# Kernel tuning notes

Hardware: AMD Instinct MI355X
Metric: run time of the kernel (lower is better)

## Reference

```python
import jax, jax.numpy as jnp
import numpy as np

BN_EPS = 1e-5


def setup_inputs() -> dict:
    key = jax.random.key(0)
    k1, k2, k3, k4 = jax.random.split(key, 4)
    B, C_in, T, V = 64, 64, 300, 25
    K, C_out = 3, 64
    x = jax.random.normal(k1, (B, C_in, T, V), dtype=jnp.float32)
    # 1x1 Conv2d weight collapsed to (K*C_out, C_in); bias (K*C_out,)
    W = jax.random.normal(k2, (K * C_out, C_in), dtype=jnp.float32) * (1.0 / np.sqrt(C_in))
    b = jax.random.normal(k3, (K * C_out,), dtype=jnp.float32) * 0.02
    A = jax.random.uniform(k4, (K, V, V), dtype=jnp.float32)
    gamma = jnp.ones((C_out,), dtype=jnp.float32)
    beta = jnp.zeros((C_out,), dtype=jnp.float32)
    return {"x": x, "W": W, "b": b, "A": A, "gamma": gamma, "beta": beta}


def reference(x, W, b, A, gamma, beta):
    B, C_in, T, V = x.shape
    K = A.shape[0]
    C_out = W.shape[0] // K
    # 1x1 conv == per-pixel matmul over channels
    x_conv = jnp.einsum('bctv,oc->botv', x, W) + b[None, :, None, None]
    # split into K partitions: (B, K, C_out, T, V)
    x_conv = x_conv.reshape(B, K, C_out, T, V)
    # fused per-partition graph matmul + sum over partitions
    out = jnp.einsum('bkctv,kvw->bctw', x_conv, A)
    # BatchNorm2d (training mode: batch statistics over B, T, V)
    mean = jnp.mean(out, axis=(0, 2, 3), keepdims=True)
    var = jnp.var(out, axis=(0, 2, 3), keepdims=True)  # biased variance
    out_hat = (out - mean) * jax.lax.rsqrt(var + BN_EPS)
    return out_hat * gamma[None, :, None, None] + beta[None, :, None, None]
```

## Files before the change

kernel.cpp:

```cpp
#include <hip/hip_runtime.h>
#include <stdint.h>


#define TT 3
#define NPIX (TT * 25)
#define NT1 5
#define NBLK 6400
#define XSTRIDE 68
#define TSZ 4800

typedef short bf16x8 __attribute__((ext_vector_type(8)));
typedef float f32x4 __attribute__((ext_vector_type(4)));

union frag_u { bf16x8 v; uint32_t u[4]; };

__device__ inline short f2bf(float f) {
    union { float f; uint32_t u; } v; v.f = f;
    uint32_t u = v.u;
    u += 0x7fffu + ((u >> 16) & 1u);
    return (short)(u >> 16);
}

__device__ inline uint32_t cvtpk(float lo, float hi) {
    uint32_t d;
    asm("v_cvt_pk_bf16_f32 %0, %1, %2" : "=v"(d) : "v"(lo), "v"(hi));
    return d;
}

__device__ inline short f2h(float f) {
    union { _Float16 h; short s; } u; u.h = (_Float16)f; return u.s;
}
__device__ inline float h2f(short s) {
    union { short s; _Float16 h; } u; u.s = s; return (float)u.h;
}

__global__ __launch_bounds__(256, 4) void sgc_main(
    const float* __restrict__ x, const float* __restrict__ W,
    const float* __restrict__ bias, const float* __restrict__ A,
    short* __restrict__ ws, float* __restrict__ stats_part)
{
    __shared__ __align__(16) short smem[18432];
    float* xT   = (float*)smem;
    short* Ylds = smem;

    const int tid  = threadIdx.x;
    const int lane = tid & 63;
    const int wave = tid >> 6;
    const int q4   = lane >> 4;
    const int wl   = lane & 15;
    const int bid  = blockIdx.x;
    const int b    = bid / 100;
    const int t0   = (bid % 100) * TT;

    bf16x8 wfrag[3][2];
    #pragma unroll
    for (int k = 0; k < 3; ++k) {
        int o = k * 64 + wave * 16 + wl;
        #pragma unroll
        for (int kb = 0; kb < 2; ++kb) {
            int ci0 = kb * 32 + q4 * 8;
            const float4 f0 = *(const float4*)&W[o * 64 + ci0];
            const float4 f1 = *(const float4*)&W[o * 64 + ci0 + 4];
            frag_u fr;
            fr.u[0] = cvtpk(f0.x, f0.y);
            fr.u[1] = cvtpk(f0.z, f0.w);
            fr.u[2] = cvtpk(f1.x, f1.y);
            fr.u[3] = cvtpk(f1.z, f1.w);
            wfrag[k][kb] = fr.v;
        }
    }

    {
        const float* xg = x + (size_t)b * 480000 + (size_t)t0 * 25 + lane * 7500;
        float4 vv[5];
        int segs[5];
        #pragma unroll
        for (int j = 0; j < 5; ++j) {
            int seg = wave + 4 * j;
            segs[j] = seg;
            if (seg < 18) {
                vv[j] = *(const float4*)(xg + seg * 4);
            } else if (seg == 18) {
                vv[j].x = xg[72]; vv[j].y = xg[73]; vv[j].z = xg[74]; vv[j].w = 0.f;
            }
        }
        #pragma unroll
        for (int j = 0; j < 5; ++j) {
            int seg = segs[j];
            if (seg < 19) {
                int px0 = seg * 4;
                xT[(px0 + 0) * XSTRIDE + lane] = vv[j].x;
                xT[(px0 + 1) * XSTRIDE + lane] = vv[j].y;
                xT[(px0 + 2) * XSTRIDE + lane] = vv[j].z;
                if (seg < 18) xT[(px0 + 3) * XSTRIDE + lane] = vv[j].w;
            }
        }
    }

    __syncthreads();

    f32x4 acc[3][NT1];
    #pragma unroll
    for (int k = 0; k < 3; ++k)
        #pragma unroll
        for (int nt = 0; nt < NT1; ++nt) {
            f32x4 zf = {0.f, 0.f, 0.f, 0.f};
            acc[k][nt] = zf;
        }

    #pragma unroll
    for (int nt = 0; nt < NT1; ++nt) {
        int px = nt * 16 + wl;
        if (px > 74) px = 74;
        const float* row = &xT[px * XSTRIDE + q4 * 8];
        float4 q0 = *(const float4*)&row[0];
        float4 q1 = *(const float4*)&row[4];
        float4 q2 = *(const float4*)&row[32];
        float4 q3 = *(const float4*)&row[36];
        frag_u x0, x1;
        x0.u[0] = cvtpk(q0.x, q0.y); x0.u[1] = cvtpk(q0.z, q0.w);
        x0.u[2] = cvtpk(q1.x, q1.y); x0.u[3] = cvtpk(q1.z, q1.w);
        x1.u[0] = cvtpk(q2.x, q2.y); x1.u[1] = cvtpk(q2.z, q2.w);
        x1.u[2] = cvtpk(q3.x, q3.y); x1.u[3] = cvtpk(q3.z, q3.w);
        #pragma unroll
        for (int k = 0; k < 3; ++k) {
            acc[k][nt] = __builtin_amdgcn_mfma_f32_16x16x32_bf16(
                wfrag[k][0], x0.v, acc[k][nt], 0, 0, 0);
            acc[k][nt] = __builtin_amdgcn_mfma_f32_16x16x32_bf16(
                wfrag[k][1], x1.v, acc[k][nt], 0, 0, 0);
        }
    }

    __syncthreads();

    const int wbase = wave * 4608;

    #pragma unroll
    for (int tile = 0; tile < 9; ++tile)
        *(int*)&Ylds[wbase + tile * 512 + 384 + lane * 2] = 0;

    float4 bv[3];
    #pragma unroll
    for (int k = 0; k < 3; ++k)
        bv[k] = *(const float4*)&bias[k * 64 + wave * 16 + q4 * 4];

    #pragma unroll
    for (int nt = 0; nt < NT1; ++nt) {
        int n = nt * 16 + wl;
        if (n < NPIX) {
            int t = n / 25, v = n - t * 25;
            #pragma unroll
            for (int k = 0; k < 3; ++k) {
                int base = wbase + (t * 3 + k) * 512
                         + (v >> 3) * 128 + q4 * 32 + (v & 7);
                const float* bp = (const float*)&bv[k];
                #pragma unroll
                for (int r = 0; r < 4; ++r)
                    Ylds[base + r * 8] = f2bf(acc[k][nt][r] + bp[r]);
            }
        }
    }

    bf16x8 bfrag2[2][3];
    #pragma unroll
    for (int nt2 = 0; nt2 < 2; ++nt2) {
        int w = nt2 * 16 + wl;
        #pragma unroll
        for (int kb2 = 0; kb2 < 3; ++kb2) {
            frag_u fr;
            #pragma unroll
            for (int p = 0; p < 4; ++p) {
                int v0 = q4 * 8 + 2 * p;
                float a0 = (w < 25 && v0     < 25) ? A[(kb2 * 25 + v0) * 25 + w]     : 0.f;
                float a1 = (w < 25 && v0 + 1 < 25) ? A[(kb2 * 25 + v0 + 1) * 25 + w] : 0.f;
                fr.u[p] = cvtpk(a0, a1);
            }
            bfrag2[nt2][kb2] = fr.v;
        }
    }

    float ssum[4] = {0.f, 0.f, 0.f, 0.f};
    float ssq[4]  = {0.f, 0.f, 0.f, 0.f};
    short* wstile = ws + (size_t)bid * TSZ;
    const int cl0 = q4 * 4;
    const int c0  = wave * 16 + cl0;

    #pragma unroll
    for (int t = 0; t < TT; ++t) {
        bf16x8 a2[3];
        #pragma unroll
        for (int kb2 = 0; kb2 < 3; ++kb2)
            a2[kb2] = *(const bf16x8*)&Ylds[wbase + (t * 3 + kb2) * 512 + lane * 8];

        f32x4 acc2[2];
        #pragma unroll
        for (int nt2 = 0; nt2 < 2; ++nt2) {
            f32x4 zf = {0.f, 0.f, 0.f, 0.f};
            acc2[nt2] = zf;
            #pragma unroll
            for (int kb2 = 0; kb2 < 3; ++kb2)
                acc2[nt2] = __builtin_amdgcn_mfma_f32_16x16x32_bf16(
                    a2[kb2], bfrag2[nt2][kb2], acc2[nt2], 0, 0, 0);
        }

        #pragma unroll
        for (int nt2 = 0; nt2 < 2; ++nt2) {
            int w = nt2 * 16 + wl;
            bool valid = (w < 25);
            #pragma unroll
            for (int r = 0; r < 4; ++r) {
                float val = acc2[nt2][r];
                if (valid) {
                    wstile[(c0 + r) * 75 + t * 25 + w] = f2h(val);
                    ssum[r] += val;
                    ssq[r]  += val * val;
                }
            }
        }
    }

    #pragma unroll
    for (int r = 0; r < 4; ++r) {
        float s = ssum[r], q = ssq[r];
        #pragma unroll
        for (int d = 1; d < 16; d <<= 1) {
            s += __shfl_xor(s, d);
            q += __shfl_xor(q, d);
        }
        if (wl == 0) {
            int c = c0 + r;
            int slot = bid & 63;
            atomicAdd(&stats_part[slot * 128 + c], s);
            atomicAdd(&stats_part[slot * 128 + 64 + c], q);
        }
    }
}

__global__ void sgc_finalize(const float* __restrict__ stats_part,
                             const float* __restrict__ gamma,
                             const float* __restrict__ beta,
                             float* __restrict__ scaleshift)
{
    int c = threadIdx.x;
    float s = 0.f, q = 0.f;
    #pragma unroll 8
    for (int slot = 0; slot < 64; ++slot) {
        s += stats_part[slot * 128 + c];
        q += stats_part[slot * 128 + 64 + c];
    }
    const float invN = 1.f / 480000.f;
    float mean = s * invN;
    float var  = q * invN - mean * mean;
    float rstd = rsqrtf(var + 1e-5f);
    float sc = rstd * gamma[c];
    scaleshift[c]      = sc;
    scaleshift[64 + c] = beta[c] - mean * sc;
}

__global__ __launch_bounds__(256) void sgc_normws(
    const short* __restrict__ ws, const float* __restrict__ scaleshift,
    float* __restrict__ out)
{
    const int bid   = blockIdx.x;
    const int b     = bid / 100;
    const int chunk = bid % 100;
    const short* tile = ws + (size_t)bid * TSZ;
    float* ob = out + (size_t)b * 480000 + (size_t)chunk * NPIX;

    #pragma unroll
    for (int j = 0; j < 19; ++j) {
        int i = threadIdx.x + 256 * j;
        if (i < 4800) {
            int c = i / 75;
            int r = i - c * 75;
            float y = h2f(tile[i]);
            ob[c * 7500 + r] = y * scaleshift[c] + scaleshift[64 + c];
        }
    }
}

__global__ __launch_bounds__(256, 3) void sgc_main_fb(
    const float* __restrict__ x, const float* __restrict__ W,
    const float* __restrict__ bias, const float* __restrict__ A,
    float* __restrict__ out, float* __restrict__ stats_part)
{
    __shared__ __align__(16) short Ylds[18432];
    __shared__ __align__(16) short Acat[3072];

    const int tid  = threadIdx.x;
    const int lane = tid & 63;
    const int wave = tid >> 6;
    const int q4   = lane >> 4;
    const int wl   = lane & 15;
    const int bid  = blockIdx.x;
    const int b    = bid / 100;
    const int t0   = (bid % 100) * TT;

    {
        bf16x8 z8 = {0,0,0,0,0,0,0,0};
        #pragma unroll
        for (int j = 0; j < 3; ++j) {
            int s = tid + 256 * j;
            if (s < 576)
                *(bf16x8*)&Ylds[(s >> 4) * 512 + 384 + (s & 15) * 8] = z8;
        }
    }

    #pragma unroll
    for (int j = 0; j < 2; ++j) {
        int g = tid + 256 * j;
        if (g < 384) {
            int tile = g >> 6;
            int kb2  = tile >> 1, nt2 = tile & 1;
            int oct  = (g >> 4) & 3;
            int w    = nt2 * 16 + (g & 15);
            frag_u fr;
            #pragma unroll
            for (int p = 0; p < 4; ++p) {
                int v0 = oct * 8 + 2 * p;
                float a0 = (w < 25 && v0     < 25) ? A[(kb2 * 25 + v0) * 25 + w]     : 0.f;
                float a1 = (w < 25 && v0 + 1 < 25) ? A[(kb2 * 25 + v0 + 1) * 25 + w] : 0.f;
                fr.u[p] = cvtpk(a0, a1);
            }
            *(bf16x8*)&Acat[g * 8] = fr.v;
        }
    }

    bf16x8 wfrag[3][2];
    #pragma unroll
    for (int mti = 0; mti < 3; ++mti) {
        int o = (wave * 3 + mti) * 16 + wl;
        #pragma unroll
        for (int kb = 0; kb < 2; ++kb) {
            int ci0 = kb * 32 + q4 * 8;
            const float4 f0 = *(const float4*)&W[o * 64 + ci0];
            const float4 f1 = *(const float4*)&W[o * 64 + ci0 + 4];
            frag_u fr;
            fr.u[0] = cvtpk(f0.x, f0.y);
            fr.u[1] = cvtpk(f0.z, f0.w);
            fr.u[2] = cvtpk(f1.x, f1.y);
            fr.u[3] = cvtpk(f1.z, f1.w);
            wfrag[mti][kb] = fr.v;
        }
    }

    const float* xp = x + (size_t)b * 480000 + (size_t)t0 * 25;
    f32x4 acc[3][NT1];
    #pragma unroll
    for (int mti = 0; mti < 3; ++mti)
        #pragma unroll
        for (int nt = 0; nt < NT1; ++nt) {
            f32x4 zf = {0.f, 0.f, 0.f, 0.f};
            acc[mti][nt] = zf;
        }

    #pragma unroll
    for (int nt = 0; nt < NT1; ++nt) {
        int n = nt * 16 + wl;
        if (n > NPIX - 1) n = NPIX - 1;
        int loff = q4 * 60000 + n;
        bf16x8 xb[2];
        #pragma unroll
        for (int kb = 0; kb < 2; ++kb) {
            float xv[8];
            #pragma unroll
            for (int jj = 0; jj < 8; ++jj)
                xv[jj] = (xp + (kb * 32 + jj) * 7500)[loff];
            frag_u fr;
            #pragma unroll
            for (int p = 0; p < 4; ++p)
                fr.u[p] = cvtpk(xv[2 * p], xv[2 * p + 1]);
            xb[kb] = fr.v;
        }
        #pragma unroll
        for (int mti = 0; mti < 3; ++mti) {
            acc[mti][nt] = __builtin_amdgcn_mfma_f32_16x16x32_bf16(
                wfrag[mti][0], xb[0], acc[mti][nt], 0, 0, 0);
            acc[mti][nt] = __builtin_amdgcn_mfma_f32_16x16x32_bf16(
                wfrag[mti][1], xb[1], acc[mti][nt], 0, 0, 0);
        }
    }

    float4 bv[3];
    #pragma unroll
    for (int mti = 0; mti < 3; ++mti)
        bv[mti] = *(const float4*)&bias[(wave * 3 + mti) * 16 + q4 * 4];

    __syncthreads();

    #pragma unroll
    for (int nt = 0; nt < NT1; ++nt) {
        int n = nt * 16 + wl;
        if (n < NPIX) {
            int t = n / 25, v = n % 25;
            #pragma unroll
            for (int mti = 0; mti < 3; ++mti) {
                int wt = wave * 3 + mti;
                int k  = wt >> 2, cq = wt & 3;
                int kv = k * 32 + v;
                int sbase = ((t * 4 + cq) * 3 + k) * 512
                          + ((kv >> 3) & 3) * 128 + q4 * 32 + (kv & 7);
                const float* bp = (const float*)&bv[mti];
                #pragma unroll
                for (int r = 0; r < 4; ++r)
                    Ylds[sbase + r * 8] = f2bf(acc[mti][nt][r] + bp[r]);
            }
        }
    }
    __syncthreads();

    bf16x8 bfrag2[2][3];
    #pragma unroll
    for (int nt2 = 0; nt2 < 2; ++nt2)
        #pragma unroll
        for (int kb2 = 0; kb2 < 3; ++kb2)
            bfrag2[nt2][kb2] = *(const bf16x8*)&Acat[((kb2 * 2 + nt2) * 64 + lane) * 8];

    float ssum[4] = {0.f, 0.f, 0.f, 0.f};
    float ssq[4]  = {0.f, 0.f, 0.f, 0.f};
    const int c0 = wave * 16 + q4 * 4;

    #pragma unroll
    for (int t = 0; t < TT; ++t) {
        bf16x8 a2[3];
        #pragma unroll
        for (int kb2 = 0; kb2 < 3; ++kb2)
            a2[kb2] = *(const bf16x8*)&Ylds[(((t * 4 + wave) * 3 + kb2) * 64 + lane) * 8];

        f32x4 acc2[2];
        #pragma unroll
        for (int nt2 = 0; nt2 < 2; ++nt2) {
            f32x4 zf = {0.f, 0.f, 0.f, 0.f};
            acc2[nt2] = zf;
            #pragma unroll
            for (int kb2 = 0; kb2 < 3; ++kb2)
                acc2[nt2] = __builtin_amdgcn_mfma_f32_16x16x32_bf16(
                    a2[kb2], bfrag2[nt2][kb2], acc2[nt2], 0, 0, 0);
        }

        #pragma unroll
        for (int nt2 = 0; nt2 < 2; ++nt2) {
            int w = nt2 * 16 + wl;
            bool valid = (w < 25);
            #pragma unroll
            for (int r = 0; r < 4; ++r) {
                float val = acc2[nt2][r];
                if (valid) {
                    out[(size_t)((b * 64 + c0 + r) * 300 + t0 + t) * 25 + w] = val;
                    ssum[r] += val;
                    ssq[r]  += val * val;
                }
            }
        }
    }

    #pragma unroll
    for (int r = 0; r < 4; ++r) {
        float s = ssum[r], q = ssq[r];
        #pragma unroll
        for (int d = 1; d < 16; d <<= 1) {
            s += __shfl_xor(s, d);
            q += __shfl_xor(q, d);
        }
        if (wl == 0) {
            int c = c0 + r;
            int slot = bid & 63;
            atomicAdd(&stats_part[slot * 128 + c], s);
            atomicAdd(&stats_part[slot * 128 + 64 + c], q);
        }
    }
}

__global__ __launch_bounds__(256) void sgc_norm_fb(float* __restrict__ out,
                                                   const float* __restrict__ scaleshift)
{
    const int total4 = 30720000 / 4;
    int stride = gridDim.x * 256;
    for (int i = blockIdx.x * 256 + threadIdx.x; i < total4; i += stride) {
        int c = (i / 1875) & 63;
        float sc = scaleshift[c], sh = scaleshift[64 + c];
        float4 v = *((float4*)out + i);
        v.x = v.x * sc + sh;
        v.y = v.y * sc + sh;
        v.z = v.z * sc + sh;
        v.w = v.w * sc + sh;
        *((float4*)out + i) = v;
    }
}

extern "C" void kernel_launch(void* const* d_in, const int* in_sizes, int n_in,
                              void* d_out, int out_size, void* d_ws, size_t ws_size,
                              hipStream_t stream)
{
    const float* x     = (const float*)d_in[0];
    const float* W     = (const float*)d_in[1];
    const float* bias  = (const float*)d_in[2];
    const float* A     = (const float*)d_in[3];
    const float* gamma = (const float*)d_in[4];
    const float* beta  = (const float*)d_in[5];
    float* out = (float*)d_out;

    const size_t tile_bytes = (size_t)NBLK * TSZ * sizeof(short);
    const size_t need = tile_bytes + 64 * 128 * sizeof(float) + 128 * sizeof(float);

    if (ws_size >= need) {
        short* tiles      = (short*)d_ws;
        float* stats      = (float*)((char*)d_ws + tile_bytes);
        float* scaleshift = stats + 64 * 128;

        hipMemsetAsync(stats, 0, 64 * 128 * sizeof(float), stream);
        sgc_main<<<NBLK, 256, 0, stream>>>(x, W, bias, A, tiles, stats);
        sgc_finalize<<<1, 64, 0, stream>>>(stats, gamma, beta, scaleshift);
        sgc_normws<<<NBLK, 256, 0, stream>>>(tiles, scaleshift, out);
    } else {
        float* stats      = (float*)d_ws;
        float* scaleshift = stats + 64 * 128;

        hipMemsetAsync(stats, 0, 64 * 128 * sizeof(float), stream);
        sgc_main_fb<<<NBLK, 256, 0, stream>>>(x, W, bias, A, out, stats);
        sgc_finalize<<<1, 64, 0, stream>>>(stats, gamma, beta, scaleshift);
        sgc_norm_fb<<<4096, 256, 0, stream>>>(out, scaleshift);
    }
}
```

Before: 344.2 us.

## Fuse conv, graph matmul, BN stats and normalize into one cooperative persistent kernel

Replaces the three-kernel pipeline (main, finalize, normalize) plus memset with a single cooperative kernel of 1024 persistent blocks. Each block loops over tiles, prefetching the next tile's x into registers while computing the current one. Per-block BN partial sums are written without atomics, then reduced after a grid sync, and a second grid sync precedes the in-kernel normalization pass. This removes launch overhead and atomics, but adds two grid-wide barriers and a normalize phase whose fp16 workspace reads are strided. The fallback path now writes into a workspace region that may be too small, since it runs exactly when ws_size is below the requirement.

Result: slower. 941.6 us (+173.6%).

```diff
diff --git a/kernel.cpp b/kernel.cpp
--- a/kernel.cpp
+++ b/kernel.cpp
@@ -1,11 +1,15 @@
 #include <hip/hip_runtime.h>
+#include <hip/hip_cooperative_groups.h>
 #include <stdint.h>
+
+namespace cg = cooperative_groups;
 
 
 #define TT 3
 #define NPIX (TT * 25)
 #define NT1 5
-#define NBLK 6400
+#define NTILE 6400
+#define GRID 1024
 #define XSTRIDE 68
 #define TSZ 4800
 
@@ -34,10 +38,12 @@
     union { short s; _Float16 h; } u; u.s = s; return (float)u.h;
 }
 
-__global__ __launch_bounds__(256, 4) void sgc_main(
+__global__ __launch_bounds__(256, 4) void sgc_fused(
     const float* __restrict__ x, const float* __restrict__ W,
     const float* __restrict__ bias, const float* __restrict__ A,
-    short* __restrict__ ws, float* __restrict__ stats_part)
+    const float* __restrict__ gamma, const float* __restrict__ beta,
+    float* __restrict__ out, short* __restrict__ ws,
+    float* __restrict__ stats_part, float* __restrict__ chansum)
 {
     __shared__ __align__(16) short smem[18432];
     float* xT   = (float*)smem;
@@ -49,8 +55,6 @@
     const int q4   = lane >> 4;
     const int wl   = lane & 15;
     const int bid  = blockIdx.x;
-    const int b    = bid / 100;
-    const int t0   = (bid % 100) * TT;
 
     bf16x8 wfrag[3][2];
     #pragma unroll
@@ -70,23 +74,53 @@
         }
     }
 
+    bf16x8 bfrag2[2][3];
+    #pragma unroll
+    for (int nt2 = 0; nt2 < 2; ++nt2) {
+        int w = nt2 * 16 + wl;
+        #pragma unroll
+        for (int kb2 = 0; kb2 < 3; ++kb2) {
+            frag_u fr;
+            #pragma unroll
+            for (int p = 0; p < 4; ++p) {
+                int v0 = q4 * 8 + 2 * p;
+                float a0 = (w < 25 && v0     < 25) ? A[(kb2 * 25 + v0) * 25 + w]     : 0.f;
+                float a1 = (w < 25 && v0 + 1 < 25) ? A[(kb2 * 25 + v0 + 1) * 25 + w] : 0.f;
+                fr.u[p] = cvtpk(a0, a1);
+            }
+            bfrag2[nt2][kb2] = fr.v;
+        }
+    }
+
+    float4 bv[3];
+    #pragma unroll
+    for (int k = 0; k < 3; ++k)
+        bv[k] = *(const float4*)&bias[k * 64 + wave * 16 + q4 * 4];
+
+    float ssum[4] = {0.f, 0.f, 0.f, 0.f};
+    float ssq[4]  = {0.f, 0.f, 0.f, 0.f};
+    const int c0 = wave * 16 + q4 * 4;
+
+    float4 vv[5];
     {
+        int tile = bid;
+        int b = tile / 100;
+        int t0 = (tile - b * 100) * TT;
         const float* xg = x + (size_t)b * 480000 + (size_t)t0 * 25 + lane * 7500;
-        float4 vv[5];
-        int segs[5];
         #pragma unroll
         for (int j = 0; j < 5; ++j) {
             int seg = wave + 4 * j;
-            segs[j] = seg;
-            if (seg < 18) {
-                vv[j] = *(const float4*)(xg + seg * 4);
-            } else if (seg == 18) {
-                vv[j].x = xg[72]; vv[j].y = xg[73]; vv[j].z = xg[74]; vv[j].w = 0.f;
-            }
-        }
+            if (seg < 18) vv[j] = *(const float4*)(xg + seg * 4);
+            else if (seg == 18) { vv[j].x = xg[72]; vv[j].y = xg[73]; vv[j].z = xg[74]; vv[j].w = 0.f; }
+        }
+    }
+
+    for (int tile = bid; tile < NTILE; tile += GRID) {
+        __syncthreads();
+
         #pragma unroll
         for (int j = 0; j < 5; ++j) {
-            int seg = segs[j];
+            int seg = wave + 4 * j;
             if (seg < 19) {
                 int px0 = seg * 4;
                 xT[(px0 + 0) * XSTRIDE + lane] = vv[j].x;
@@ -95,8 +129,246 @@
                 if (seg < 18) xT[(px0 + 3) * XSTRIDE + lane] = vv[j].w;
             }
         }
-    }
-
+
+        float4 vv2[5];
+        int ntile = tile + GRID;
+        if (ntile < NTILE) {
+            int b2 = ntile / 100;
+            int t02 = (ntile - b2 * 100) * TT;
+            const float* xg = x + (size_t)b2 * 480000 + (size_t)t02 * 25 + lane * 7500;
+            #pragma unroll
+            for (int j = 0; j < 5; ++j) {
+                int seg = wave + 4 * j;
+                if (seg < 18) vv2[j] = *(const float4*)(xg + seg * 4);
+                else if (seg == 18) { vv2[j].x = xg[72]; vv2[j].y = xg[73]; vv2[j].z = xg[74]; vv2[j].w = 0.f; }
+            }
+        }
+
+        __syncthreads();
+
+        f32x4 acc[3][NT1];
+        #pragma unroll
+        for (int k = 0; k < 3; ++k)
+            #pragma unroll
+            for (int nt = 0; nt < NT1; ++nt) {
+                f32x4 zf = {0.f, 0.f, 0.f, 0.f};
+                acc[k][nt] = zf;
+            }
+
+        #pragma unroll
+        for (int nt = 0; nt < NT1; ++nt) {
+            int px = nt * 16 + wl;
+            if (px > 74) px = 74;
+            const float* row = &xT[px * XSTRIDE + q4 * 8];
+            float4 a0 = *(const float4*)&row[0];
+            float4 a1 = *(const float4*)&row[4];
+            float4 a2 = *(const float4*)&row[32];
+            float4 a3 = *(const float4*)&row[36];
+            frag_u x0, x1;
+            x0.u[0] = cvtpk(a0.x, a0.y); x0.u[1] = cvtpk(a0.z, a0.w);
+            x0.u[2] = cvtpk(a1.x, a1.y); x0.u[3] = cvtpk(a1.z, a1.w);
+            x1.u[0] = cvtpk(a2.x, a2.y); x1.u[1] = cvtpk(a2.z, a2.w);
+            x1.u[2] = cvtpk(a3.x, a3.y); x1.u[3] = cvtpk(a3.z, a3.w);
+            #pragma unroll
+            for (int k = 0; k < 3; ++k) {
+                acc[k][nt] = __builtin_amdgcn_mfma_f32_16x16x32_bf16(
+                    wfrag[k][0], x0.v, acc[k][nt], 0, 0, 0);
+                acc[k][nt] = __builtin_amdgcn_mfma_f32_16x16x32_bf16(
+                    wfrag[k][1], x1.v, acc[k][nt], 0, 0, 0);
+            }
+        }
+
+        __syncthreads();
+
+        const int wbase = wave * 4608;
+
+        #pragma unroll
+        for (int tl = 0; tl < 9; ++tl)
+            *(int*)&Ylds[wbase + tl * 512 + 384 + lane * 2] = 0;
+
+        #pragma unroll
+        for (int nt = 0; nt < NT1; ++nt) {
+            int n = nt * 16 + wl;
+            if (n < NPIX) {
+                int t = n / 25, v = n - t * 25;
+                #pragma unroll
+                for (int k = 0; k < 3; ++k) {
+                    int base = wbase + (t * 3 + k) * 512
+                             + (v >> 3) * 128 + q4 * 32 + (v & 7);
+                    const float* bp = (const float*)&bv[k];
+                    #pragma unroll
+                    for (int r = 0; r < 4; ++r)
+                        Ylds[base + r * 8] = f2bf(acc[k][nt][r] + bp[r]);
+                }
+            }
+        }
+
+        short* wstile = ws + (size_t)tile * TSZ;
+        #pragma unroll
+        for (int t = 0; t < TT; ++t) {
+            bf16x8 a2[3];
+            #pragma unroll
+            for (int kb2 = 0; kb2 < 3; ++kb2)
+                a2[kb2] = *(const bf16x8*)&Ylds[wbase + (t * 3 + kb2) * 512 + lane * 8];
+
+            f32x4 acc2[2];
+            #pragma unroll
+            for (int nt2 = 0; nt2 < 2; ++nt2) {
+                f32x4 zf = {0.f, 0.f, 0.f, 0.f};
+                acc2[nt2] = zf;
+                #pragma unroll
+                for (int kb2 = 0; kb2 < 3; ++kb2)
+                    acc2[nt2] = __builtin_amdgcn_mfma_f32_16x16x32_bf16(
+                        a2[kb2], bfrag2[nt2][kb2], acc2[nt2], 0, 0, 0);
+            }
+
+            #pragma unroll
+            for (int nt2 = 0; nt2 < 2; ++nt2) {
+                int w = nt2 * 16 + wl;
+                bool valid = (w < 25);
+                #pragma unroll
+                for (int r = 0; r < 4; ++r) {
+                    float val = acc2[nt2][r];
+                    if (valid) {
+                        wstile[(c0 + r) * 75 + t * 25 + w] = f2h(val);
+                        ssum[r] += val;
+                        ssq[r]  += val * val;
+                    }
+                }
+            }
+        }
+
+        #pragma unroll
+        for (int j = 0; j < 5; ++j) vv[j] = vv2[j];
+    }
+
+    #pragma unroll
+    for (int r = 0; r < 4; ++r) {
+        float s = ssum[r], q = ssq[r];
+        #pragma unroll
+        for (int d = 1; d < 16; d <<= 1) {
+            s += __shfl_xor(s, d);
+            q += __shfl_xor(q, d);
+        }
+        if (wl == 0) {
+            stats_part[bid * 128 + c0 + r]      = s;
+            stats_part[bid * 128 + 64 + c0 + r] = q;
+        }
+    }
+
+    __threadfence();
+    cg::this_grid().sync();
+
+    if (bid < 64) {
+        float* red = (float*)smem;
+        int m  = 2 * bid + (tid >> 7);
+        int ts = tid & 127;
+        float s = 0.f;
+        #pragma unroll
+        for (int k = 0; k < 8; ++k)
+            s += stats_part[(ts * 8 + k) * 128 + m];
+        red[tid] = s;
+        __syncthreads();
+        #pragma unroll
+        for (int d = 64; d > 0; d >>= 1) {
+            if ((tid & 127) < d) red[tid] += red[tid + d];
+            __syncthreads();
+        }
+        if ((tid & 127) == 0) chansum[m] = red[tid];
+    }
+
+    __threadfence();
+    cg::this_grid().sync();
+
+    const float invN = 1.f / 480000.f;
+    const int Rbase = bid * 4;
+    #pragma unroll
+    for (int rr = 0; rr < 4; ++rr) {
+        int R = Rbase + rr;
+        int b = R >> 6, c = R & 63;
+        float mean = chansum[c] * invN;
+        float var  = chansum[64 + c] * invN - mean * mean;
+        float rstd = rsqrtf(var + 1e-5f);
+        float sc = rstd * gamma[c];
+        float sh = beta[c] - mean * sc;
+        const short* wrow = ws + (size_t)(b * 100) * TSZ + c * 75;
+        float* orow = out + (size_t)b * 480000 + (size_t)c * 7500;
+        #pragma unroll
+        for (int kk = 0; kk < 8; ++kk) {
+            int p4 = tid + 256 * kk;
+            if (p4 < 1875) {
+                int p = p4 * 4;
+                float4 v;
+                #pragma unroll
+                for (int j = 0; j < 4; ++j) {
+                    int pj = p + j;
+                    int ch = pj / 75;
+                    int r  = pj - ch * 75;
+                    ((float*)&v)[j] = h2f(wrow[ch * TSZ + r]) * sc + sh;
+                }
+                *(float4*)&orow[p] = v;
+            }
+        }
+    }
+}
+
+__global__ __launch_bounds__(256, 4) void sgc_main_v4(
+    const float* __restrict__ x, const float* __restrict__ W,
+    const float* __restrict__ bias, const float* __restrict__ A,
+    short* __restrict__ ws, float* __restrict__ stats_part)
+{
+    __shared__ __align__(16) short smem[18432];
+    float* xT   = (float*)smem;
+    short* Ylds = smem;
+
+    const int tid  = threadIdx.x;
+    const int lane = tid & 63;
+    const int wave = tid >> 6;
+    const int q4   = lane >> 4;
+    const int wl   = lane & 15;
+    const int bid  = blockIdx.x;
+    const int b    = bid / 100;
+    const int t0   = (bid % 100) * TT;
+
+    bf16x8 wfrag[3][2];
+    #pragma unroll
+    for (int k = 0; k < 3; ++k) {
+        int o = k * 64 + wave * 16 + wl;
+        #pragma unroll
+        for (int kb = 0; kb < 2; ++kb) {
+            int ci0 = kb * 32 + q4 * 8;
+            const float4 f0 = *(const float4*)&W[o * 64 + ci0];
+            const float4 f1 = *(const float4*)&W[o * 64 + ci0 + 4];
+            frag_u fr;
+            fr.u[0] = cvtpk(f0.x, f0.y);
+            fr.u[1] = cvtpk(f0.z, f0.w);
+            fr.u[2] = cvtpk(f1.x, f1.y);
+            fr.u[3] = cvtpk(f1.z, f1.w);
+            wfrag[k][kb] = fr.v;
+        }
+    }
+
+    {
+        const float* xg = x + (size_t)b * 480000 + (size_t)t0 * 25 + lane * 7500;
+        float4 vv[5];
+        #pragma unroll
+        for (int j = 0; j < 5; ++j) {
+            int seg = wave + 4 * j;
+            if (seg < 18) vv[j] = *(const float4*)(xg + seg * 4);
+            else if (seg == 18) { vv[j].x = xg[72]; vv[j].y = xg[73]; vv[j].z = xg[74]; vv[j].w = 0.f; }
+        }
+        #pragma unroll
+        for (int j = 0; j < 5; ++j) {
+            int seg = wave + 4 * j;
+            if (seg < 19) {
+                int px0 = seg * 4;
+                xT[(px0 + 0) * XSTRIDE + lane] = vv[j].x;
+                xT[(px0 + 1) * XSTRIDE + lane] = vv[j].y;
+                xT[(px0 + 2) * XSTRIDE + lane] = vv[j].z;
+                if (seg < 18) xT[(px0 + 3) * XSTRIDE + lane] = vv[j].w;
+            }
+        }
+    }
     __syncthreads();
 
     f32x4 acc[3][NT1];
@@ -113,15 +385,15 @@
         int px = nt * 16 + wl;
         if (px > 74) px = 74;
         const float* row = &xT[px * XSTRIDE + q4 * 8];
-        float4 q0 = *(const float4*)&row[0];
-        float4 q1 = *(const float4*)&row[4];
-        float4 q2 = *(const float4*)&row[32];
-        float4 q3 = *(const float4*)&row[36];
+        float4 a0 = *(const float4*)&row[0];
+        float4 a1 = *(const float4*)&row[4];
+        float4 a2 = *(const float4*)&row[32];
+        float4 a3 = *(const float4*)&row[36];
         frag_u x0, x1;
-        x0.u[0] = cvtpk(q0.x, q0.y); x0.u[1] = cvtpk(q0.z, q0.w);
-        x0.u[2] = cvtpk(q1.x, q1.y); x0.u[3] = cvtpk(q1.z, q1.w);
-        x1.u[0] = cvtpk(q2.x, q2.y); x1.u[1] = cvtpk(q2.z, q2.w);
-        x1.u[2] = cvtpk(q3.x, q3.y); x1.u[3] = cvtpk(q3.z, q3.w);
+        x0.u[0] = cvtpk(a0.x, a0.y); x0.u[1] = cvtpk(a0.z, a0.w);
+        x0.u[2] = cvtpk(a1.x, a1.y); x0.u[3] = cvtpk(a1.z, a1.w);
+        x1.u[0] = cvtpk(a2.x, a2.y); x1.u[1] = cvtpk(a2.z, a2.w);
+        x1.u[2] = cvtpk(a3.x, a3.y); x1.u[3] = cvtpk(a3.z, a3.w);
         #pragma unroll
         for (int k = 0; k < 3; ++k) {
             acc[k][nt] = __builtin_amdgcn_mfma_f32_16x16x32_bf16(
@@ -130,14 +402,12 @@
                 wfrag[k][1], x1.v, acc[k][nt], 0, 0, 0);
         }
     }
-
     __syncthreads();
 
     const int wbase = wave * 4608;
-
-    #pragma unroll
-    for (int tile = 0; tile < 9; ++tile)
-        *(int*)&Ylds[wbase + tile * 512 + 384 + lane * 2] = 0;
+    #pragma unroll
+    for (int tl = 0; tl < 9; ++tl)
+        *(int*)&Ylds[wbase + tl * 512 + 384 + lane * 2] = 0;
 
     float4 bv[3];
     #pragma unroll
@@ -182,8 +452,7 @@
     float ssum[4] = {0.f, 0.f, 0.f, 0.f};
     float ssq[4]  = {0.f, 0.f, 0.f, 0.f};
     short* wstile = ws + (size_t)bid * TSZ;
-    const int cl0 = q4 * 4;
-    const int c0  = wave * 16 + cl0;
+    const int c0  = wave * 16 + q4 * 4;
 
     #pragma unroll
     for (int t = 0; t < TT; ++t) {
@@ -279,215 +548,6 @@
     }
 }
 
-__global__ __launch_bounds__(256, 3) void sgc_main_fb(
-    const float* __restrict__ x, const float* __restrict__ W,
-    const float* __restrict__ bias, const float* __restrict__ A,
-    float* __restrict__ out, float* __restrict__ stats_part)
-{
-    __shared__ __align__(16) short Ylds[18432];
-    __shared__ __align__(16) short Acat[3072];
-
-    const int tid  = threadIdx.x;
-    const int lane = tid & 63;
-    const int wave = tid >> 6;
-    const int q4   = lane >> 4;
-    const int wl   = lane & 15;
-    const int bid  = blockIdx.x;
-    const int b    = bid / 100;
-    const int t0   = (bid % 100) * TT;
-
-    {
-        bf16x8 z8 = {0,0,0,0,0,0,0,0};
-        #pragma unroll
-        for (int j = 0; j < 3; ++j) {
-            int s = tid + 256 * j;
-            if (s < 576)
-                *(bf16x8*)&Ylds[(s >> 4) * 512 + 384 + (s & 15) * 8] = z8;
-        }
-    }
-
-    #pragma unroll
-    for (int j = 0; j < 2; ++j) {
-        int g = tid + 256 * j;
-        if (g < 384) {
-            int tile = g >> 6;
-            int kb2  = tile >> 1, nt2 = tile & 1;
-            int oct  = (g >> 4) & 3;
-            int w    = nt2 * 16 + (g & 15);
-            frag_u fr;
-            #pragma unroll
-            for (int p = 0; p < 4; ++p) {
-                int v0 = oct * 8 + 2 * p;
-                float a0 = (w < 25 && v0     < 25) ? A[(kb2 * 25 + v0) * 25 + w]     : 0.f;
-                float a1 = (w < 25 && v0 + 1 < 25) ? A[(kb2 * 25 + v0 + 1) * 25 + w] : 0.f;
-                fr.u[p] = cvtpk(a0, a1);
-            }
-            *(bf16x8*)&Acat[g * 8] = fr.v;
-        }
-    }
-
-    bf16x8 wfrag[3][2];
-    #pragma unroll
-    for (int mti = 0; mti < 3; ++mti) {
-        int o = (wave * 3 + mti) * 16 + wl;
-        #pragma unroll
-        for (int kb = 0; kb < 2; ++kb) {
-            int ci0 = kb * 32 + q4 * 8;
-            const float4 f0 = *(const float4*)&W[o * 64 + ci0];
-            const float4 f1 = *(const float4*)&W[o * 64 + ci0 + 4];
-            frag_u fr;
-            fr.u[0] = cvtpk(f0.x, f0.y);
-            fr.u[1] = cvtpk(f0.z, f0.w);
-            fr.u[2] = cvtpk(f1.x, f1.y);
-            fr.u[3] = cvtpk(f1.z, f1.w);
-            wfrag[mti][kb] = fr.v;
-        }
-    }
-
-    const float* xp = x + (size_t)b * 480000 + (size_t)t0 * 25;
-    f32x4 acc[3][NT1];
-    #pragma unroll
-    for (int mti = 0; mti < 3; ++mti)
-        #pragma unroll
-        for (int nt = 0; nt < NT1; ++nt) {
-            f32x4 zf = {0.f, 0.f, 0.f, 0.f};
-            acc[mti][nt] = zf;
-        }
-
-    #pragma unroll
-    for (int nt = 0; nt < NT1; ++nt) {
-        int n = nt * 16 + wl;
-        if (n > NPIX - 1) n = NPIX - 1;
-        int loff = q4 * 60000 + n;
-        bf16x8 xb[2];
-        #pragma unroll
-        for (int kb = 0; kb < 2; ++kb) {
-            float xv[8];
-            #pragma unroll
-            for (int jj = 0; jj < 8; ++jj)
-                xv[jj] = (xp + (kb * 32 + jj) * 7500)[loff];
-            frag_u fr;
-            #pragma unroll
-            for (int p = 0; p < 4; ++p)
-                fr.u[p] = cvtpk(xv[2 * p], xv[2 * p + 1]);
-            xb[kb] = fr.v;
-        }
-        #pragma unroll
-        for (int mti = 0; mti < 3; ++mti) {
-            acc[mti][nt] = __builtin_amdgcn_mfma_f32_16x16x32_bf16(
-                wfrag[mti][0], xb[0], acc[mti][nt], 0, 0, 0);
-            acc[mti][nt] = __builtin_amdgcn_mfma_f32_16x16x32_bf16(
-                wfrag[mti][1], xb[1], acc[mti][nt], 0, 0, 0);
-        }
-    }
-
-    float4 bv[3];
-    #pragma unroll
-    for (int mti = 0; mti < 3; ++mti)
-        bv[mti] = *(const float4*)&bias[(wave * 3 + mti) * 16 + q4 * 4];
-
-    __syncthreads();
-
-    #pragma unroll
-    for (int nt = 0; nt < NT1; ++nt) {
-        int n = nt * 16 + wl;
-        if (n < NPIX) {
-            int t = n / 25, v = n % 25;
-            #pragma unroll
-            for (int mti = 0; mti < 3; ++mti) {
-                int wt = wave * 3 + mti;
-                int k  = wt >> 2, cq = wt & 3;
-                int kv = k * 32 + v;
-                int sbase = ((t * 4 + cq) * 3 + k) * 512
-                          + ((kv >> 3) & 3) * 128 + q4 * 32 + (kv & 7);
-                const float* bp = (const float*)&bv[mti];
-                #pragma unroll
-                for (int r = 0; r < 4; ++r)
-                    Ylds[sbase + r * 8] = f2bf(acc[mti][nt][r] + bp[r]);
-            }
-        }
-    }
-    __syncthreads();
-
-    bf16x8 bfrag2[2][3];
-    #pragma unroll
-    for (int nt2 = 0; nt2 < 2; ++nt2)
-        #pragma unroll
-        for (int kb2 = 0; kb2 < 3; ++kb2)
-            bfrag2[nt2][kb2] = *(const bf16x8*)&Acat[((kb2 * 2 + nt2) * 64 + lane) * 8];
-
-    float ssum[4] = {0.f, 0.f, 0.f, 0.f};
-    float ssq[4]  = {0.f, 0.f, 0.f, 0.f};
-    const int c0 = wave * 16 + q4 * 4;
-
-    #pragma unroll
-    for (int t = 0; t < TT; ++t) {
-        bf16x8 a2[3];
-        #pragma unroll
-        for (int kb2 = 0; kb2 < 3; ++kb2)
-            a2[kb2] = *(const bf16x8*)&Ylds[(((t * 4 + wave) * 3 + kb2) * 64 + lane) * 8];
-
-        f32x4 acc2[2];
-        #pragma unroll
-        for (int nt2 = 0; nt2 < 2; ++nt2) {
-            f32x4 zf = {0.f, 0.f, 0.f, 0.f};
-            acc2[nt2] = zf;
-            #pragma unroll
-            for (int kb2 = 0; kb2 < 3; ++kb2)
-                acc2[nt2] = __builtin_amdgcn_mfma_f32_16x16x32_bf16(
-                    a2[kb2], bfrag2[nt2][kb2], acc2[nt2], 0, 0, 0);
-        }
-
-        #pragma unroll
-        for (int nt2 = 0; nt2 < 2; ++nt2) {
-            int w = nt2 * 16 + wl;
-            bool valid = (w < 25);
-            #pragma unroll
-            for (int r = 0; r < 4; ++r) {
-                float val = acc2[nt2][r];
-                if (valid) {
-                    out[(size_t)((b * 64 + c0 + r) * 300 + t0 + t) * 25 + w] = val;
-                    ssum[r] += val;
-                    ssq[r]  += val * val;
-                }
-            }
-        }
-    }
-
-    #pragma unroll
-    for (int r = 0; r < 4; ++r) {
-        float s = ssum[r], q = ssq[r];
-        #pragma unroll
-        for (int d = 1; d < 16; d <<= 1) {
-            s += __shfl_xor(s, d);
-            q += __shfl_xor(q, d);
-        }
-        if (wl == 0) {
-            int c = c0 + r;
-            int slot = bid & 63;
-            atomicAdd(&stats_part[slot * 128 + c], s);
-            atomicAdd(&stats_part[slot * 128 + 64 + c], q);
-        }
-    }
-}
-
-__global__ __launch_bounds__(256) void sgc_norm_fb(float* __restrict__ out,
-                                                   const float* __restrict__ scaleshift)
-{
-    const int total4 = 30720000 / 4;
-    int stride = gridDim.x * 256;
-    for (int i = blockIdx.x * 256 + threadIdx.x; i < total4; i += stride) {
-        int c = (i / 1875) & 63;
-        float sc = scaleshift[c], sh = scaleshift[64 + c];
-        float4 v = *((float4*)out + i);
-        v.x = v.x * sc + sh;
-        v.y = v.y * sc + sh;
-        v.z = v.z * sc + sh;
-        v.w = v.w * sc + sh;
-        *((float4*)out + i) = v;
-    }
-}
-
 extern "C" void kernel_launch(void* const* d_in, const int* in_sizes, int n_in,
                               void* d_out, int out_size, void* d_ws, size_t ws_size,
                               hipStream_t stream)
@@ -500,25 +560,34 @@
     const float* beta  = (const float*)d_in[5];
     float* out = (float*)d_out;
 
-    const size_t tile_bytes = (size_t)NBLK * TSZ * sizeof(short);
-    const size_t need = tile_bytes + 64 * 128 * sizeof(float) + 128 * sizeof(float);
+    const size_t tile_bytes = (size_t)NTILE * TSZ * sizeof(short);
+    const size_t stat_bytes = (size_t)GRID * 128 * sizeof(float);
+    const size_t need = tile_bytes + stat_bytes + 128 * sizeof(float);
 
     if (ws_size >= need) {
         short* tiles      = (short*)d_ws;
         float* stats      = (float*)((char*)d_ws + tile_bytes);
-        float* scaleshift = stats + 64 * 128;
-
-        hipMemsetAsync(stats, 0, 64 * 128 * sizeof(float), stream);
-        sgc_main<<<NBLK, 256, 0, stream>>>(x, W, bias, A, tiles, stats);
-        sgc_finalize<<<1, 64, 0, stream>>>(stats, gamma, beta, scaleshift);
-        sgc_normws<<<NBLK, 256, 0, stream>>>(tiles, scaleshift, out);
+        float* chansum    = stats + GRID * 128;
+
+        void* args[] = { (void*)&x, (void*)&W, (void*)&bias, (void*)&A,
+                         (void*)&gamma, (void*)&beta, (void*)&out,
+                         (void*)&tiles, (void*)&stats, (void*)&chansum };
+        hipError_t e = hipLaunchCooperativeKernel(
+            (const void*)sgc_fused, dim3(GRID), dim3(256), args, 0, stream);
+
+        if (e != hipSuccess) {
+            hipMemsetAsync(stats, 0, 64 * 128 * sizeof(float), stream);
+            sgc_main_v4<<<NTILE, 256, 0, stream>>>(x, W, bias, A, tiles, stats);
+            sgc_finalize<<<1, 64, 0, stream>>>(stats, gamma, beta, chansum);
+            sgc_normws<<<NTILE, 256, 0, stream>>>(tiles, chansum, out);
+        }
     } else {
         float* stats      = (float*)d_ws;
         float* scaleshift = stats + 64 * 128;
-
+        short* tiles = (short*)(scaleshift + 128);
         hipMemsetAsync(stats, 0, 64 * 128 * sizeof(float), stream);
-        sgc_main_fb<<<NBLK, 256, 0, stream>>>(x, W, bias, A, out, stats);
+        sgc_main_v4<<<NTILE, 256, 0, stream>>>(x, W, bias, A, tiles, stats);
         sgc_finalize<<<1, 64, 0, stream>>>(stats, gamma, beta, scaleshift);
-        sgc_norm_fb<<<4096, 256, 0, stream>>>(out, scaleshift);
-    }
-}
+        sgc_normws<<<NTILE, 256, 0, stream>>>(tiles, scaleshift, out);
+    }
+}
```
